# Optimization experiments

Hardware: AMD Instinct MI355X
Metric: run time of the kernel (lower is better)

The kernel has to match this reference:

```python
import jax, jax.numpy as jnp
import numpy as np

OBS_RADIUS = 1.0
N = 8192      # num_agents
IN_DIM = 4    # state dim: [x, y, vx, vy]
HID = 64


def setup_inputs() -> dict:
    key = jax.random.key(0)
    ks = jax.random.split(key, 6)
    states = jax.random.normal(ks[0], (N, IN_DIM), dtype=jnp.float32)
    W1 = jax.random.normal(ks[1], (IN_DIM, HID), dtype=jnp.float32) / np.sqrt(IN_DIM).astype(np.float32)
    b1 = jnp.zeros((HID,), jnp.float32)
    W2 = jax.random.normal(ks[2], (HID, HID), dtype=jnp.float32) / np.sqrt(HID).astype(np.float32)
    b2 = jnp.zeros((HID,), jnp.float32)
    cw = jax.random.normal(ks[3], (HID,), dtype=jnp.float32) / np.sqrt(HID).astype(np.float32)  # Conv1d(64,1,1) weight
    cb = jnp.zeros((1,), jnp.float32)
    return {"states": states, "W1": W1, "b1": b1, "W2": W2, "b2": b2, "cw": cw, "cb": cb}


def _build_norm_adj(states):
    # radius graph on first two coords (positions); no self edges in the edge list,
    # GCNConv then adds self-loops and does symmetric D^-1/2 (A+I) D^-1/2 normalization.
    pos = states[:, :2]
    d2 = jnp.sum((pos[:, None, :] - pos[None, :, :]) ** 2, axis=-1)  # [N, N]
    mask = d2 <= jnp.asarray(OBS_RADIUS ** 2, states.dtype)          # [N, N] bool (incl. diagonal)
    eye = jnp.eye(N, dtype=bool)
    A_hat = jnp.where(mask & ~eye, jnp.asarray(1.0, states.dtype), 0.0) + jnp.eye(N, dtype=states.dtype)
    dinv = jax.lax.rsqrt(jnp.sum(A_hat, axis=1))                     # deg >= 1 (self loop)
    A_norm = dinv[:, None] * A_hat * dinv[None, :]
    return A_norm, mask


def reference(states, W1, b1, W2, b2, cw, cb):
    A_norm, mask = _build_norm_adj(states)
    # GCNConv 1: aggregate(normalized adj) of X W, plus bias, ReLU
    h = jax.nn.relu(A_norm @ (states @ W1) + b1)   # [N, 64]
    # GCNConv 2
    h = jax.nn.relu(A_norm @ (h @ W2) + b2)        # [N, 64]
    # Conv1d(64 -> 1, kernel=1): pointwise linear over channels
    out = h @ cw[:, None] + cb                     # [N, 1]
    return out, mask
```

## Files before the change

### kernel.cpp

```cpp
#include <hip/hip_runtime.h>
#include <hip/hip_bf16.h>
#include <stdint.h>

#define NPTS 8192
#define KSPLIT 8

typedef float f32x4 __attribute__((ext_vector_type(4)));
typedef short s16x8 __attribute__((ext_vector_type(8)));

__device__ __forceinline__ unsigned short f2bf(float f) {
    unsigned int u = __builtin_bit_cast(unsigned int, f);
    u += 0x7FFFu + ((u >> 16) & 1u);
    return (unsigned short)(u >> 16);
}


__global__ __launch_bounds__(256) void k_mask(const float* __restrict__ states,
                                              float* __restrict__ mout,
                                              unsigned long long* __restrict__ maskb,
                                              float* __restrict__ dinv) {
    __shared__ float2 xy[NPTS];
    int tid = threadIdx.x;
    for (int r = tid; r < NPTS; r += 256) {
        float4 s = ((const float4*)states)[r];
        xy[r] = make_float2(s.x, s.y);
    }
    __syncthreads();
    int wv = tid >> 6, L = tid & 63;
    int rowbase = blockIdx.x * 16 + wv * 4;
    for (int rr = 0; rr < 4; ++rr) {
        int i = rowbase + rr;
        float2 pi = xy[i];
        int deg = 0;
        float* orow = mout + (size_t)i * NPTS;
        unsigned long long* brow = maskb + (size_t)i * 128;
        for (int it = 0; it < 128; ++it) {
            int j = it * 64 + L;
            float2 pj = xy[j];
            float dx = pi.x - pj.x;
            float dy = pi.y - pj.y;
            float d2 = __fadd_rn(__fmul_rn(dx, dx), __fmul_rn(dy, dy));
            bool pred = (d2 <= 1.0f);
            orow[j] = pred ? 1.0f : 0.0f;
            unsigned long long b = __ballot(pred);
            if (L == 0) brow[it] = b;
            deg += (int)__popcll(b);
        }
        if (L == 0) dinv[i] = rsqrtf((float)deg);
    }
}

__global__ __launch_bounds__(256) void k_y1(const float* __restrict__ states,
                                            const float* __restrict__ W1,
                                            const float* __restrict__ dinv,
                                            uint4* __restrict__ y) {
    int gid = blockIdx.x * 256 + threadIdx.x;
    int L = gid & 63, ct = (gid >> 6) & 3, kb = gid >> 8;
    int n = L & 15, quad = L >> 4;
    int col = ct * 16 + n;
    float w0 = W1[col], w1 = W1[64 + col], w2 = W1[128 + col], w3 = W1[192 + col];
    unsigned short frag[8];
#pragma unroll
    for (int t = 0; t < 8; ++t) {
        int k = kb * 32 + quad * 8 + t;
        float4 s = ((const float4*)states)[k];
        float acc = s.x * w0 + s.y * w1 + s.z * w2 + s.w * w3;
        frag[t] = f2bf(dinv[k] * acc);
    }
    uint4 u;
    u.x = (unsigned)frag[0] | ((unsigned)frag[1] << 16);
    u.y = (unsigned)frag[2] | ((unsigned)frag[3] << 16);
    u.z = (unsigned)frag[4] | ((unsigned)frag[5] << 16);
    u.w = (unsigned)frag[6] | ((unsigned)frag[7] << 16);
    y[gid] = u;
}

__global__ __launch_bounds__(256, 4) void k_agg(const uint4* __restrict__ y,
                                                const unsigned int* __restrict__ maskb,
                                                float* __restrict__ zp) {
    int tid = threadIdx.x;
    int wv = tid >> 6, L = tid & 63;
    int bid = blockIdx.x;
    int mt = bid >> 3, ks = bid & (KSPLIT - 1);
    int n = L & 15, quad = L >> 4;
    int i = mt * 64 + wv * 16 + n;
    const unsigned int* mrow = maskb + (size_t)i * 256 + ks * 32;
    const uint4* yb = y + (size_t)(ks * 32) * 256 + L;

    f32x4 acc[4] = {{0,0,0,0},{0,0,0,0},{0,0,0,0},{0,0,0,0}};
    uint4 bcur[4];
    unsigned int mw = mrow[0];
#pragma unroll
    for (int ct = 0; ct < 4; ++ct) bcur[ct] = yb[ct * 64];

    for (int kb = 0; kb < 32; ++kb) {
        uint4 bnext[4]; unsigned int mwn = 0;
        if (kb < 31) {
            const uint4* p = yb + (kb + 1) * 256;
#pragma unroll
            for (int ct = 0; ct < 4; ++ct) bnext[ct] = p[ct * 64];
            mwn = mrow[kb + 1];
        }
        unsigned int byte = (mw >> (quad * 8)) & 0xFFu;
        s16x8 a;
#pragma unroll
        for (int t = 0; t < 8; ++t)
            a[t] = (short)(((byte >> t) & 1u) ? 0x3F80 : 0);
#pragma unroll
        for (int ct = 0; ct < 4; ++ct)
            acc[ct] = __builtin_amdgcn_mfma_f32_16x16x32_bf16(
                a, __builtin_bit_cast(s16x8, bcur[ct]), acc[ct], 0, 0, 0);
#pragma unroll
        for (int ct = 0; ct < 4; ++ct) bcur[ct] = bnext[ct];
        mw = mwn;
    }
    float* zb = zp + (size_t)ks * (NPTS * 64) + (size_t)(mt * 64 + wv * 16) * 64;
#pragma unroll
    for (int ct = 0; ct < 4; ++ct)
#pragma unroll
        for (int r = 0; r < 4; ++r)
            zb[(quad * 4 + r) * 64 + ct * 16 + n] = acc[ct][r];
}

__global__ __launch_bounds__(256) void k_h1y2(const float* __restrict__ zp,
                                              const float* __restrict__ dinv,
                                              const float* __restrict__ b1,
                                              const float* __restrict__ W2,
                                              uint4* __restrict__ y2) {
    __shared__ float w2s[4096];
    __shared__ float hbuf[8 * 64];
    __shared__ unsigned short ybuf[8 * 64];
    int tid = threadIdx.x;
#pragma unroll
    for (int s = 0; s < 16; ++s) w2s[s * 256 + tid] = W2[s * 256 + tid];
    int j0 = blockIdx.x * 8;
#pragma unroll
    for (int e = tid; e < 512; e += 256) {
        int r = e >> 6, c = e & 63;
        int j = j0 + r;
        float z = 0.0f;
#pragma unroll
        for (int s = 0; s < KSPLIT; ++s) z += zp[(size_t)s * (NPTS * 64) + j * 64 + c];
        hbuf[r * 64 + c] = fmaxf(dinv[j] * z + b1[c], 0.0f);
    }
    __syncthreads();
#pragma unroll
    for (int e = tid; e < 512; e += 256) {
        int r = e >> 6, c = e & 63;
        const float* hr = hbuf + r * 64;
        float acc = 0.0f;
#pragma unroll
        for (int m = 0; m < 64; ++m) acc = fmaf(hr[m], w2s[m * 64 + c], acc);
        ybuf[r * 64 + c] = f2bf(dinv[j0 + r] * acc);
    }
    __syncthreads();
    if (tid < 64) {
        int c = tid;
        unsigned short v[8];
#pragma unroll
        for (int r = 0; r < 8; ++r) v[r] = ybuf[r * 64 + c];
        uint4 u;
        u.x = (unsigned)v[0] | ((unsigned)v[1] << 16);
        u.y = (unsigned)v[2] | ((unsigned)v[3] << 16);
        u.z = (unsigned)v[4] | ((unsigned)v[5] << 16);
        u.w = (unsigned)v[6] | ((unsigned)v[7] << 16);
        int kb = j0 >> 5, quad = (j0 >> 3) & 3, ct = c >> 4, nn = c & 15;
        y2[(kb * 4 + ct) * 64 + quad * 16 + nn] = u;
    }
}

__global__ __launch_bounds__(256) void k_out(const float* __restrict__ zp,
                                             const float* __restrict__ dinv,
                                             const float* __restrict__ b2,
                                             const float* __restrict__ cw,
                                             const float* __restrict__ cb,
                                             float* __restrict__ out) {
    int tid = threadIdx.x;
    int wv = tid >> 6, L = tid & 63;
    int i = blockIdx.x * 4 + wv;
    int idx = i * 64 + L;
    float z = 0.0f;
#pragma unroll
    for (int s = 0; s < KSPLIT; ++s) z += zp[(size_t)s * (NPTS * 64) + idx];
    float h = fmaxf(dinv[i] * z + b2[L], 0.0f);
    float v = h * cw[L];
#pragma unroll
    for (int off = 32; off > 0; off >>= 1) v += __shfl_down(v, off, 64);
    if (L == 0) out[i] = v + cb[0];
}

extern "C" void kernel_launch(void* const* d_in, const int* in_sizes, int n_in,
                              void* d_out, int out_size, void* d_ws, size_t ws_size,
                              hipStream_t stream) {
    const float* states = (const float*)d_in[0];
    const float* W1 = (const float*)d_in[1];
    const float* b1 = (const float*)d_in[2];
    const float* W2 = (const float*)d_in[3];
    const float* b2 = (const float*)d_in[4];
    const float* cw = (const float*)d_in[5];
    const float* cb = (const float*)d_in[6];
    float* out = (float*)d_out;
    float* mout = out + NPTS;

    char* ws = (char*)d_ws;
    float* dinv               = (float*)(ws);
    unsigned long long* maskb = (unsigned long long*)(ws + (1 << 16));
    uint4* y1                 = (uint4*)(ws + (1 << 16) + (8 << 20));
    uint4* y2                 = (uint4*)(ws + (1 << 16) + (9 << 20));
    float* zp                 = (float*)(ws + (1 << 16) + (10 << 20));

    hipLaunchKernelGGL(k_mask, dim3(512), dim3(256), 0, stream, states, mout, maskb, dinv);
    hipLaunchKernelGGL(k_y1,   dim3(256), dim3(256), 0, stream, states, W1, dinv, y1);
    hipLaunchKernelGGL(k_agg,  dim3(128 * KSPLIT), dim3(256), 0, stream,
                       y1, (const unsigned int*)maskb, zp);
    hipLaunchKernelGGL(k_h1y2, dim3(1024), dim3(256), 0, stream, zp, dinv, b1, W2, y2);
    hipLaunchKernelGGL(k_agg,  dim3(128 * KSPLIT), dim3(256), 0, stream,
                       y2, (const unsigned int*)maskb, zp);
    hipLaunchKernelGGL(k_out,  dim3(2048), dim3(256), 0, stream, zp, dinv, b2, cw, cb, out);
}
```

Measured before the change: 378.9 us.

## Double rows per wave in aggregation and use nontemporal mask stores

Each wave in the aggregation kernel now computes two 16-row tiles, so every loaded B fragment of y feeds two MFMAs. This halves the block count and the global traffic for y per output row. The dense float mask output is written with nontemporal stores so the 256 MB write stream bypasses cache. The trade-off is more registers per wave and half as many blocks (512) to spread across the CUs.

```diff
diff --git a/kernel.cpp b/kernel.cpp
--- a/kernel.cpp
+++ b/kernel.cpp
@@ -41,7 +41,7 @@
             float dy = pi.y - pj.y;
             float d2 = __fadd_rn(__fmul_rn(dx, dx), __fmul_rn(dy, dy));
             bool pred = (d2 <= 1.0f);
-            orow[j] = pred ? 1.0f : 0.0f;
+            __builtin_nontemporal_store(pred ? 1.0f : 0.0f, &orow[j]);
             unsigned long long b = __ballot(pred);
             if (L == 0) brow[it] = b;
             deg += (int)__popcll(b);
@@ -75,51 +75,61 @@
     y[gid] = u;
 }
 
-__global__ __launch_bounds__(256, 4) void k_agg(const uint4* __restrict__ y,
-                                                const unsigned int* __restrict__ maskb,
-                                                float* __restrict__ zp) {
+__global__ __launch_bounds__(256) void k_agg(const uint4* __restrict__ y,
+                                             const unsigned int* __restrict__ maskb,
+                                             float* __restrict__ zp) {
     int tid = threadIdx.x;
     int wv = tid >> 6, L = tid & 63;
     int bid = blockIdx.x;
     int mt = bid >> 3, ks = bid & (KSPLIT - 1);
     int n = L & 15, quad = L >> 4;
-    int i = mt * 64 + wv * 16 + n;
-    const unsigned int* mrow = maskb + (size_t)i * 256 + ks * 32;
+    int i0 = mt * 128 + wv * 32 + n;
+    const unsigned int* mrow0 = maskb + (size_t)i0 * 256 + ks * 32;
+    const unsigned int* mrow1 = mrow0 + 16 * 256;
     const uint4* yb = y + (size_t)(ks * 32) * 256 + L;
 
-    f32x4 acc[4] = {{0,0,0,0},{0,0,0,0},{0,0,0,0},{0,0,0,0}};
+    f32x4 acc[2][4] = {{{0,0,0,0},{0,0,0,0},{0,0,0,0},{0,0,0,0}},
+                       {{0,0,0,0},{0,0,0,0},{0,0,0,0},{0,0,0,0}}};
     uint4 bcur[4];
-    unsigned int mw = mrow[0];
+    unsigned int mw0 = mrow0[0], mw1 = mrow1[0];
 #pragma unroll
     for (int ct = 0; ct < 4; ++ct) bcur[ct] = yb[ct * 64];
 
     for (int kb = 0; kb < 32; ++kb) {
-        uint4 bnext[4]; unsigned int mwn = 0;
+        uint4 bnext[4]; unsigned int mwn0 = 0, mwn1 = 0;
         if (kb < 31) {
             const uint4* p = yb + (kb + 1) * 256;
 #pragma unroll
             for (int ct = 0; ct < 4; ++ct) bnext[ct] = p[ct * 64];
-            mwn = mrow[kb + 1];
-        }
-        unsigned int byte = (mw >> (quad * 8)) & 0xFFu;
-        s16x8 a;
-#pragma unroll
-        for (int t = 0; t < 8; ++t)
-            a[t] = (short)(((byte >> t) & 1u) ? 0x3F80 : 0);
+            mwn0 = mrow0[kb + 1];
+            mwn1 = mrow1[kb + 1];
+        }
+        unsigned int byte0 = (mw0 >> (quad * 8)) & 0xFFu;
+        unsigned int byte1 = (mw1 >> (quad * 8)) & 0xFFu;
+        s16x8 a0, a1;
+#pragma unroll
+        for (int t = 0; t < 8; ++t) {
+            a0[t] = (short)(((byte0 >> t) & 1u) ? 0x3F80 : 0);
+            a1[t] = (short)(((byte1 >> t) & 1u) ? 0x3F80 : 0);
+        }
+#pragma unroll
+        for (int ct = 0; ct < 4; ++ct) {
+            s16x8 b = __builtin_bit_cast(s16x8, bcur[ct]);
+            acc[0][ct] = __builtin_amdgcn_mfma_f32_16x16x32_bf16(a0, b, acc[0][ct], 0, 0, 0);
+            acc[1][ct] = __builtin_amdgcn_mfma_f32_16x16x32_bf16(a1, b, acc[1][ct], 0, 0, 0);
+        }
+#pragma unroll
+        for (int ct = 0; ct < 4; ++ct) bcur[ct] = bnext[ct];
+        mw0 = mwn0; mw1 = mwn1;
+    }
+    float* zb = zp + (size_t)ks * (NPTS * 64) + (size_t)(mt * 128 + wv * 32) * 64;
+#pragma unroll
+    for (int g = 0; g < 2; ++g)
 #pragma unroll
         for (int ct = 0; ct < 4; ++ct)
-            acc[ct] = __builtin_amdgcn_mfma_f32_16x16x32_bf16(
-                a, __builtin_bit_cast(s16x8, bcur[ct]), acc[ct], 0, 0, 0);
-#pragma unroll
-        for (int ct = 0; ct < 4; ++ct) bcur[ct] = bnext[ct];
-        mw = mwn;
-    }
-    float* zb = zp + (size_t)ks * (NPTS * 64) + (size_t)(mt * 64 + wv * 16) * 64;
-#pragma unroll
-    for (int ct = 0; ct < 4; ++ct)
-#pragma unroll
-        for (int r = 0; r < 4; ++r)
-            zb[(quad * 4 + r) * 64 + ct * 16 + n] = acc[ct][r];
+#pragma unroll
+            for (int r = 0; r < 4; ++r)
+                zb[(g * 16 + quad * 4 + r) * 64 + ct * 16 + n] = acc[g][ct][r];
 }
 
 __global__ __launch_bounds__(256) void k_h1y2(const float* __restrict__ zp,
@@ -211,10 +221,10 @@
 
     hipLaunchKernelGGL(k_mask, dim3(512), dim3(256), 0, stream, states, mout, maskb, dinv);
     hipLaunchKernelGGL(k_y1,   dim3(256), dim3(256), 0, stream, states, W1, dinv, y1);
-    hipLaunchKernelGGL(k_agg,  dim3(128 * KSPLIT), dim3(256), 0, stream,
+    hipLaunchKernelGGL(k_agg,  dim3(64 * KSPLIT), dim3(256), 0, stream,
                        y1, (const unsigned int*)maskb, zp);
     hipLaunchKernelGGL(k_h1y2, dim3(1024), dim3(256), 0, stream, zp, dinv, b1, W2, y2);
-    hipLaunchKernelGGL(k_agg,  dim3(128 * KSPLIT), dim3(256), 0, stream,
+    hipLaunchKernelGGL(k_agg,  dim3(64 * KSPLIT), dim3(256), 0, stream,
                        y2, (const unsigned int*)maskb, zp);
     hipLaunchKernelGGL(k_out,  dim3(2048), dim3(256), 0, stream, zp, dinv, b2, cw, cb, out);
 }
```

Result: faster. 370.8 us (-2.1%).
